# Kernel tuning notes

Measured on AMD Instinct MI355X. Metric: run time of the kernel, lower is better.

The kernel has to match this reference:

```python
import jax, jax.numpy as jnp
import numpy as np

SEQ, B, H = 2048, 2, 4096
N_HEADS = 32
N_KV = 2
HEAD_DIM = H // N_HEADS          # 128
ROT_DIM = HEAD_DIM // 2          # 64 (rope cache last-2 dim = 32 pairs)


def setup_inputs() -> dict:
    key = jax.random.key(0)
    ks = jax.random.split(key, 8)
    hidden_states = jax.random.normal(ks[0], (SEQ, B, H), dtype=jnp.float32)
    rotary_pos_emb = jax.random.normal(ks[1], (SEQ, 1, ROT_DIM // 2, 2), dtype=jnp.float32)
    s = 0.02
    Wq = jax.random.normal(ks[2], (H, H), dtype=jnp.float32) * s
    bq = jnp.zeros((H,), dtype=jnp.float32)
    Wk = jax.random.normal(ks[3], (H, N_KV * HEAD_DIM), dtype=jnp.float32) * s
    bk = jnp.zeros((N_KV * HEAD_DIM,), dtype=jnp.float32)
    Wv = jax.random.normal(ks[4], (H, N_KV * HEAD_DIM), dtype=jnp.float32) * s
    bv = jnp.zeros((N_KV * HEAD_DIM,), dtype=jnp.float32)
    Wo = jax.random.normal(ks[5], (H, H), dtype=jnp.float32) * s
    return {"hidden_states": hidden_states, "rotary_pos_emb": rotary_pos_emb,
            "Wq": Wq, "bq": bq, "Wk": Wk, "bk": bk, "Wv": Wv, "bv": bv, "Wo": Wo}


def _apply_rope(x, rope):
    # x: [sq, b, np, hn]; rope: [sq, 1, rot/2, 2]
    sq = x.shape[0]
    rot = rope.shape[-2] * 2
    x_rot, x_pass = x[..., :rot], x[..., rot:]
    xs = x_rot.reshape(x.shape[0], x.shape[1], x.shape[2], rot // 2, 2)
    rc = rope[:sq].reshape(sq, -1, 1, rot // 2, 2)  # [sq,1,1,rot/2,2]
    o0 = xs[..., 0] * rc[..., 0] - xs[..., 1] * rc[..., 1]
    o1 = xs[..., 1] * rc[..., 0] + xs[..., 0] * rc[..., 1]
    out = jnp.stack([o0, o1], axis=-1).reshape(x_rot.shape)
    return jnp.concatenate([out, x_pass], axis=-1)


def reference(hidden_states, rotary_pos_emb, Wq, bq, Wk, bk, Wv, bv, Wo):
    sq, b, h = hidden_states.shape
    group = N_HEADS // N_KV

    q = (hidden_states @ Wq + bq).reshape(sq, b, N_HEADS, HEAD_DIM)
    k = (hidden_states @ Wk + bk).reshape(sq, b, N_KV, HEAD_DIM)
    v = (hidden_states @ Wv + bv).reshape(sq, b, N_KV, HEAD_DIM)

    q = _apply_rope(q, rotary_pos_emb)
    k = _apply_rope(k, rotary_pos_emb)

    # GQA expand: head index = kv_head * group + g (matches expand+view in torch)
    k = jnp.repeat(k, group, axis=2)  # [sq, b, N_HEADS, hd]
    v = jnp.repeat(v, group, axis=2)

    scale = 1.0 / np.sqrt(HEAD_DIM)
    scores = jnp.einsum("sbhd,tbhd->bhst", q, k) * scale  # [b, nh, sq, sq]
    causal = jnp.tril(jnp.ones((sq, sq), dtype=bool))
    scores = jnp.where(causal, scores, jnp.finfo(scores.dtype).min)
    probs = jax.nn.softmax(scores, axis=-1)
    ctx = jnp.einsum("bhst,tbhd->sbhd", probs, v)  # [sq, b, nh, hd]
    ctx = ctx.reshape(sq, b, h)
    return ctx @ Wo
```

## Files before the change

### kernel.cpp

```cpp
#include <hip/hip_runtime.h>
#include <stdint.h>

#define SEQ   2048
#define BATCH 2
#define HD    4096
#define NH    32
#define NKV   2
#define HDIM  128
#define NT    (SEQ*BATCH)
#define KVC   (NKV*HDIM)

typedef short  bf16x8 __attribute__((ext_vector_type(8)));
typedef short  sh4    __attribute__((ext_vector_type(4)));
typedef float  f32x4  __attribute__((ext_vector_type(4)));

__device__ __forceinline__ float bf2f(unsigned short u){
  union { unsigned int i; float f; } v; v.i = ((unsigned int)u) << 16; return v.f;
}
__device__ __forceinline__ unsigned short f2bf(float f){
  union { float f; unsigned int i; } v; v.f = f;
  unsigned int r = v.i + 0x7FFFu + ((v.i >> 16) & 1u);
  return (unsigned short)(r >> 16);
}
__device__ __forceinline__ unsigned int cvtpk_bf16(float lo, float hi){
  unsigned int r;
  asm("v_cvt_pk_bf16_f32 %0, %1, %2" : "=v"(r) : "v"(lo), "v"(hi));
  return r;
}

__device__ __forceinline__ void gload_lds16(const void* g, void* lds){
  __builtin_amdgcn_global_load_lds(
      (const __attribute__((address_space(1))) unsigned int*)(size_t)g,
      (__attribute__((address_space(3))) unsigned int*)(unsigned int)(size_t)lds,
      16, 0, 0);
}

__device__ __forceinline__ void BARRIER(){
  __builtin_amdgcn_sched_barrier(0);
  asm volatile("" ::: "memory");
  __builtin_amdgcn_s_barrier();
  asm volatile("" ::: "memory");
  __builtin_amdgcn_sched_barrier(0);
}
#define VMCNT(N) do { asm volatile("s_waitcnt vmcnt(" #N ")" ::: "memory"); \
                      __builtin_amdgcn_sched_barrier(0); } while(0)

__global__ void k_cast(const float* __restrict__ in, unsigned short* __restrict__ out, int n4){
  int i = blockIdx.x * blockDim.x + threadIdx.x;
  if (i >= n4) return;
  float4 v = ((const float4*)in)[i];
  ushort4 o; o.x = f2bf(v.x); o.y = f2bf(v.y); o.z = f2bf(v.z); o.w = f2bf(v.w);
  ((ushort4*)out)[i] = o;
}

__global__ void k_transpose(const float* __restrict__ W, unsigned short* __restrict__ WT,
                            int K, int N){
  __shared__ float t[32][33];
  int n0 = blockIdx.x * 32, k0 = blockIdx.y * 32;
  int tx = threadIdx.x, ty = threadIdx.y;
  t[ty][tx] = W[(size_t)(k0 + ty) * N + n0 + tx];
  __syncthreads();
  WT[(size_t)(n0 + ty) * K + k0 + tx] = f2bf(t[tx][ty]);
}

template<bool OUTF32>
__global__ __launch_bounds__(256) void k_gemm(
    const unsigned short* __restrict__ A,
    const unsigned short* __restrict__ BT,
    const float* __restrict__ bias,
    const float* __restrict__ bias2, int bsplit,
    void* __restrict__ C, int M, int N, int K)
{
  __shared__ unsigned short As[128*32];
  __shared__ unsigned short Bs[128*32];
  const int tid  = threadIdx.x;
  const int lane = tid & 63;
  const int w    = tid >> 6;
  const int l4   = lane >> 4, l15 = lane & 15;
  const int wm   = (w >> 1) * 64, wn = (w & 1) * 64;
  const size_t bm = (size_t)blockIdx.y * 128, bn = (size_t)blockIdx.x * 128;

  f32x4 acc[4][4] = {};
  const int scol = (lane & 3) * 8;

  for (int k0 = 0; k0 < K; k0 += 32) {
    #pragma unroll
    for (int j = 0; j < 2; ++j) {
      const int r = w*32 + j*16 + (lane >> 2);
      gload_lds16(A  + (bm + r) * (size_t)K + k0 + scol, As + (size_t)(w*32 + j*16) * 32);
      gload_lds16(BT + (bn + r) * (size_t)K + k0 + scol, Bs + (size_t)(w*32 + j*16) * 32);
    }
    __syncthreads();
    bf16x8 af[4], bfr[4];
    #pragma unroll
    for (int m = 0; m < 4; ++m)
      af[m] = *(const bf16x8*)(As + (wm + m*16 + l15)*32 + l4*8);
    #pragma unroll
    for (int n = 0; n < 4; ++n)
      bfr[n] = *(const bf16x8*)(Bs + (wn + n*16 + l15)*32 + l4*8);
    #pragma unroll
    for (int m = 0; m < 4; ++m)
      #pragma unroll
      for (int n = 0; n < 4; ++n)
        acc[m][n] = __builtin_amdgcn_mfma_f32_16x16x32_bf16(af[m], bfr[n], acc[m][n], 0, 0, 0);
    __syncthreads();
  }

  #pragma unroll
  for (int n = 0; n < 4; ++n) {
    const size_t col = bn + wn + n*16 + l15;
    float badd = 0.0f;
    if (bias) badd = (bias2 && (int)col >= bsplit) ? bias2[col - bsplit] : bias[col];
    #pragma unroll
    for (int m = 0; m < 4; ++m) {
      const size_t row0 = bm + wm + m*16 + l4*4;
      #pragma unroll
      for (int r = 0; r < 4; ++r) {
        float v = acc[m][n][r] + badd;
        if (OUTF32) ((float*)C)[(row0 + r) * (size_t)N + col] = v;
        else ((unsigned short*)C)[(row0 + r) * (size_t)N + col] = f2bf(v);
      }
    }
  }
}

template<bool OUTF32>
__global__ __launch_bounds__(512, 2) void k_gemm256(
    const unsigned short* __restrict__ A,
    const unsigned short* __restrict__ BT,
    const float* __restrict__ bias,
    void* __restrict__ C, int M, int N, int K)
{
  __shared__ __attribute__((aligned(16))) unsigned short As[2][16384];
  __shared__ __attribute__((aligned(16))) unsigned short Bs[2][16384];
  const int tid  = threadIdx.x;
  const int lane = tid & 63;
  const int w    = tid >> 6;
  const int c    = lane & 15, g = lane >> 4;
  const int wm   = w >> 2, wn = w & 3;

  const int nwg = (int)(gridDim.x * gridDim.y);
  int bid = (int)(blockIdx.y * gridDim.x + blockIdx.x);
  if ((nwg & 7) == 0) bid = (bid & 7) * (nwg >> 3) + (bid >> 3);
  const int bx = bid % (int)gridDim.x, by = bid / (int)gridDim.x;
  const size_t bm = (size_t)by * 256, bn = (size_t)bx * 256;

  const char* Ab = (const char*)(A  + bm * (size_t)K);
  const char* Bb = (const char*)(BT + bn * (size_t)K);
  const size_t Kb2 = (size_t)K * 2;
  const int cswz = (c & 7) << 4;

  f32x4 acc[8][4] = {};
  bf16x8 af[4][2], bfr[4][2];

#define STAGE_A(bi, h, k0) do { \
    _Pragma("unroll") \
    for (int _j = 0; _j < 2; ++_j) { \
      const int _i = _j*512 + tid; \
      const int _row = (h)*128 + (_i >> 3); \
      const int _ch  = _i & 7; \
      gload_lds16(Ab + (size_t)_row * Kb2 + (size_t)(k0)*2 + ((_ch*16) ^ ((_row & 7) << 4)), \
                  (char*)As[bi] + (h)*16384 + _j*8192 + w*1024); \
    } } while(0)
#define STAGE_B(bi, h, k0) do { \
    _Pragma("unroll") \
    for (int _j = 0; _j < 2; ++_j) { \
      const int _i = _j*512 + tid; \
      const int _row = (h)*128 + (_i >> 3); \
      const int _ch  = _i & 7; \
      gload_lds16(Bb + (size_t)_row * Kb2 + (size_t)(k0)*2 + ((_ch*16) ^ ((_row & 7) << 4)), \
                  (char*)Bs[bi] + (h)*16384 + _j*8192 + w*1024); \
    } } while(0)
#define LDA(bi, mg) do { \
    _Pragma("unroll") \
    for (int _m = 0; _m < 4; ++_m) { \
      const char* _p = (const char*)As[bi] + (size_t)(((mg)*128 + _m*32 + wm*16 + c) * 128); \
      af[_m][0] = *(const bf16x8*)(_p + (( 0 + g*16) ^ cswz)); \
      af[_m][1] = *(const bf16x8*)(_p + ((64 + g*16) ^ cswz)); \
    } } while(0)
#define LDB(bi, ng) do { \
    _Pragma("unroll") \
    for (int _n = 0; _n < 2; ++_n) { \
      const char* _p = (const char*)Bs[bi] + (size_t)((((ng)*2+_n)*64 + wn*16 + c) * 128); \
      bfr[(ng)*2+_n][0] = *(const bf16x8*)(_p + (( 0 + g*16) ^ cswz)); \
      bfr[(ng)*2+_n][1] = *(const bf16x8*)(_p + ((64 + g*16) ^ cswz)); \
    } } while(0)
#define MFMA16(mg, ng) do { \
    __builtin_amdgcn_s_setprio(1); \
    _Pragma("unroll") \
    for (int _m = 0; _m < 4; ++_m) \
      _Pragma("unroll") \
      for (int _n = 0; _n < 2; ++_n) { \
        acc[(mg)*4+_m][(ng)*2+_n] = __builtin_amdgcn_mfma_f32_16x16x32_bf16( \
            af[_m][0], bfr[(ng)*2+_n][0], acc[(mg)*4+_m][(ng)*2+_n], 0, 0, 0); \
        acc[(mg)*4+_m][(ng)*2+_n] = __builtin_amdgcn_mfma_f32_16x16x32_bf16( \
            af[_m][1], bfr[(ng)*2+_n][1], acc[(mg)*4+_m][(ng)*2+_n], 0, 0, 0); \
      } \
    __builtin_amdgcn_s_setprio(0); \
  } while(0)

  STAGE_A(0, 0, 0);
  STAGE_B(0, 0, 0);
  STAGE_B(0, 1, 0);
  STAGE_A(0, 1, 0);
  STAGE_A(1, 0, 64);
  STAGE_B(1, 0, 64);
  VMCNT(8);
  BARRIER();

  const int niter = K >> 7;
  for (int it = 0; it < niter; ++it) {
    const int kb = it*128 + 64;
    int k2 = it*128 + 128; if (k2 >= K) k2 = 0;
    int k3 = it*128 + 192; if (k3 >= K) k3 = 0;
    LDA(0, 0); LDB(0, 0);
    STAGE_A(1, 1, kb);
    BARRIER();
    MFMA16(0, 0);
    VMCNT(6);
    BARRIER();
    LDB(0, 1);
    STAGE_B(1, 1, kb);
    BARRIER();
    MFMA16(0, 1);
    BARRIER();
    LDA(0, 1);
    STAGE_A(0, 0, k2);
    BARRIER();
    MFMA16(1, 0);
    BARRIER();
    STAGE_B(0, 0, k2);
    BARRIER();
    MFMA16(1, 1);
    VMCNT(8);
    BARRIER();
    LDA(1, 0); LDB(1, 0);
    STAGE_A(0, 1, k2);
    BARRIER();
    MFMA16(0, 0);
    VMCNT(6);
    BARRIER();
    LDB(1, 1);
    STAGE_B(0, 1, k2);
    BARRIER();
    MFMA16(0, 1);
    BARRIER();
    LDA(1, 1);
    STAGE_A(1, 0, k3);
    BARRIER();
    MFMA16(1, 0);
    BARRIER();
    STAGE_B(1, 0, k3);
    BARRIER();
    MFMA16(1, 1);
    VMCNT(8);
    BARRIER();
  }

  #pragma unroll
  for (int m = 0; m < 8; ++m) {
    const size_t row0 = bm + m*32 + wm*16 + g*4;
    #pragma unroll
    for (int n = 0; n < 4; ++n) {
      const size_t col = bn + n*64 + wn*16 + c;
      const float badd = bias ? bias[col] : 0.0f;
      #pragma unroll
      for (int r = 0; r < 4; ++r) {
        float v = acc[m][n][r] + badd;
        if (OUTF32) ((float*)C)[(row0 + r) * (size_t)N + col] = v;
        else ((unsigned short*)C)[(row0 + r) * (size_t)N + col] = f2bf(v);
      }
    }
  }
#undef STAGE_A
#undef STAGE_B
#undef LDA
#undef LDB
#undef MFMA16
}

__global__ void k_rope(const unsigned short* __restrict__ In, const float* __restrict__ rope,
                       unsigned short* __restrict__ Out, int ldin, int ncols, int nslab,
                       int psh, float sc)
{
  int idx = blockIdx.x * 256 + threadIdx.x;
  int npair = ncols >> 1;
  if (idx >= NT * npair) return;
  int t = idx >> psh, pr = idx & (npair - 1);
  int colp = pr * 2, h = colp >> 7, d = colp & 127;
  int s = t >> 1, b = t & 1;
  float x0 = bf2f(In[(size_t)t * ldin + colp]);
  float x1 = bf2f(In[(size_t)t * ldin + colp + 1]);
  float o0 = x0, o1 = x1;
  if (d < 64) {
    int i2 = d >> 1;
    float cr = rope[((size_t)s * 32 + i2) * 2 + 0];
    float ci = rope[((size_t)s * 32 + i2) * 2 + 1];
    o0 = x0 * cr - x1 * ci;
    o1 = x1 * cr + x0 * ci;
  }
  size_t dst = ((size_t)(b * nslab + h) * SEQ + s) * HDIM + d;
  Out[dst]     = f2bf(o0 * sc);
  Out[dst + 1] = f2bf(o1 * sc);
}

__global__ void k_vt(const unsigned short* __restrict__ In, int ld,
                     unsigned short* __restrict__ Out){
  int idx = blockIdx.x * 256 + threadIdx.x;
  if (idx >= NT * KVC) return;
  int t = idx >> 8, cp = idx & 255;
  int kv = cp >> 7, d = cp & 127;
  int s = t >> 1, b = t & 1;
  Out[((size_t)(b * NKV + kv) * HDIM + d) * SEQ + s] = In[(size_t)t * ld + cp];
}

__global__ __launch_bounds__(256) void k_attn(
    const unsigned short* __restrict__ Q,
    const unsigned short* __restrict__ Kk,
    const unsigned short* __restrict__ Vt,
    unsigned short* __restrict__ Ctx)
{
  const int tid  = threadIdx.x;
  const int lane = tid & 63;
  const int w    = tid >> 6;
  const int g = lane >> 4, c = lane & 15;
  const int bh = blockIdx.y;
  const int b = bh >> 5, h = bh & 31;
  const int qb  = (int)(gridDim.x - 1 - blockIdx.x);
  const int qw0 = qb * 64 + w * 16;

  const unsigned short* Qb = Q  + ((size_t)(b * NH  + h)        * SEQ + qw0) * HDIM;
  const char* Kb = (const char*)(Kk + ((size_t)(b * NKV + (h >> 4)) * SEQ) * HDIM);
  const char* Vb = (const char*)(Vt + ((size_t)(b * NKV + (h >> 4)) * HDIM) * SEQ);

  __shared__ unsigned short Ks[64*128];
  __shared__ unsigned short Vs[128*64];
  __shared__ unsigned short Pl[4][16 * 72];
  unsigned short* P = Pl[w];

  bf16x8 qf[4];
  #pragma unroll
  for (int kk = 0; kk < 4; ++kk)
    qf[kk] = *(const bf16x8*)(Qb + (size_t)c * HDIM + kk*32 + g*8);

  f32x4 of[8] = {};
  float mrun = -1e30f, lrun = 0.0f;
  const int qmax = qw0 + 15;
  const int tblk = qb * 64 + 64;

  const int kr = lane >> 4, kc = lane & 15;
  const int vr = lane >> 3, vc = lane & 7;
  const int swz = (c & 7) << 4;

  for (int t0 = 0; t0 < tblk; t0 += 64) {
    #pragma unroll
    for (int j = 0; j < 4; ++j) {
      const int r = w*16 + j*4 + kr;
      gload_lds16(Kb + (size_t)(t0 + r) * 256 + ((kc*16) ^ ((r & 7) << 4)),
                  (char*)Ks + (w*16 + j*4) * 256);
    }
    #pragma unroll
    for (int j = 0; j < 4; ++j) {
      const int d = w*32 + j*8 + vr;
      gload_lds16(Vb + (size_t)d * (SEQ*2) + (size_t)t0*2 + ((vc*16) ^ ((d & 7) << 4)),
                  (char*)Vs + (w*32 + j*8) * 128);
    }
    __syncthreads();

    f32x4 st[4];
    #pragma unroll
    for (int T = 0; T < 4; ++T) {
      if (t0 + T*16 <= qmax) {
        f32x4 s = {};
        #pragma unroll
        for (int kk = 0; kk < 4; ++kk) {
          bf16x8 kf = *(const bf16x8*)((const char*)Ks + (T*16 + c)*256 + ((kk*64 + g*16) ^ swz));
          s = __builtin_amdgcn_mfma_f32_16x16x32_bf16(kf, qf[kk], s, 0, 0, 0);
        }
        #pragma unroll
        for (int r = 0; r < 4; ++r) {
          const int t = t0 + T*16 + g*4 + r;
          if (t > qw0 + c) s[r] = -1e30f;
        }
        st[T] = s;
      } else {
        st[T] = (f32x4){-1e30f, -1e30f, -1e30f, -1e30f};
      }
    }
    float mloc = -1e30f;
    #pragma unroll
    for (int T = 0; T < 4; ++T)
      #pragma unroll
      for (int r = 0; r < 4; ++r)
        mloc = fmaxf(mloc, st[T][r]);
    mloc = fmaxf(mloc, __shfl_xor(mloc, 16));
    mloc = fmaxf(mloc, __shfl_xor(mloc, 32));
    if (!__all(mloc - mrun <= 8.0f)) {
      const float mn = fmaxf(mrun, mloc);
      const float al = exp2f(mrun - mn);
      mrun = mn;
      lrun *= al;
      float alr[4];
      #pragma unroll
      for (int r = 0; r < 4; ++r) alr[r] = __shfl(al, g*4 + r);
      #pragma unroll
      for (int d8 = 0; d8 < 8; ++d8)
        #pragma unroll
        for (int r = 0; r < 4; ++r)
          of[d8][r] *= alr[r];
    }
    float ps = 0.0f;
    #pragma unroll
    for (int T = 0; T < 4; ++T) {
      const float p0 = exp2f(st[T][0] - mrun);
      const float p1 = exp2f(st[T][1] - mrun);
      const float p2 = exp2f(st[T][2] - mrun);
      const float p3 = exp2f(st[T][3] - mrun);
      ps += (p0 + p1) + (p2 + p3);
      const unsigned int w0 = cvtpk_bf16(p0, p1);
      const unsigned int w1 = cvtpk_bf16(p2, p3);
      *(uint2*)(P + c*72 + T*16 + g*4) = make_uint2(w0, w1);
    }
    ps += __shfl_xor(ps, 16);
    ps += __shfl_xor(ps, 32);
    lrun += ps;

    asm volatile("s_waitcnt lgkmcnt(0)" ::: "memory");
    __builtin_amdgcn_sched_barrier(0);

    const bf16x8 pa0 = *(const bf16x8*)(P + c*72 + g*8);
    #pragma unroll
    for (int d8 = 0; d8 < 8; ++d8) {
      bf16x8 vf = *(const bf16x8*)((const char*)Vs + (d8*16 + c)*128 + ((g*16) ^ swz));
      of[d8] = __builtin_amdgcn_mfma_f32_16x16x32_bf16(pa0, vf, of[d8], 0, 0, 0);
    }
    if (t0 + 32 <= qmax) {
      const bf16x8 pa1 = *(const bf16x8*)(P + c*72 + 32 + g*8);
      #pragma unroll
      for (int d8 = 0; d8 < 8; ++d8) {
        bf16x8 vf = *(const bf16x8*)((const char*)Vs + (d8*16 + c)*128 + ((64 + g*16) ^ swz));
        of[d8] = __builtin_amdgcn_mfma_f32_16x16x32_bf16(pa1, vf, of[d8], 0, 0, 0);
      }
    }
    __syncthreads();
  }

  float lr[4];
  #pragma unroll
  for (int r = 0; r < 4; ++r) lr[r] = 1.0f / __shfl(lrun, g*4 + r);
  #pragma unroll
  for (int d8 = 0; d8 < 8; ++d8) {
    #pragma unroll
    for (int r = 0; r < 4; ++r) {
      const int s = qw0 + g*4 + r;
      const float v = of[d8][r] * lr[r];
      Ctx[((size_t)(s * BATCH + b)) * HD + (size_t)h * HDIM + d8*16 + c] = f2bf(v);
    }
  }
}

extern "C" void kernel_launch(void* const* d_in, const int* in_sizes, int n_in,
                              void* d_out, int out_size, void* d_ws, size_t ws_size,
                              hipStream_t stream)
{
  const float* hs   = (const float*)d_in[0];
  const float* rope = (const float*)d_in[1];
  const float* Wq   = (const float*)d_in[2];
  const float* bq   = (const float*)d_in[3];
  const float* Wk   = (const float*)d_in[4];
  const float* bk   = (const float*)d_in[5];
  const float* Wv   = (const float*)d_in[6];
  const float* bv   = (const float*)d_in[7];
  const float* Wo   = (const float*)d_in[8];

  char* ws = (char*)d_ws;
  const size_t MB = (size_t)1 << 20;
  unsigned short* Xbf  = (unsigned short*)(ws);
  unsigned short* Ctx  = Xbf;
  unsigned short* WqT  = (unsigned short*)(ws + 32*MB);
  unsigned short* Qa   = WqT;
  unsigned short* WkT  = (unsigned short*)(ws + 64*MB);
  unsigned short* WvT  = (unsigned short*)(ws + 66*MB);
  unsigned short* WoT  = (unsigned short*)(ws + 68*MB);
  unsigned short* Qtmp = (unsigned short*)(ws + 100*MB);
  unsigned short* KVt  = (unsigned short*)(ws + 132*MB);
  unsigned short* Ka   = (unsigned short*)(ws + 136*MB);
  unsigned short* VTa  = (unsigned short*)(ws + 138*MB);

  k_cast<<<(NT*HD/4 + 255)/256, 256, 0, stream>>>(hs, Xbf, NT*HD/4);

  dim3 tb(32, 32);
  k_transpose<<<dim3(HD/32,  HD/32), tb, 0, stream>>>(Wq, WqT, HD, HD);
  k_transpose<<<dim3(KVC/32, HD/32), tb, 0, stream>>>(Wk, WkT, HD, KVC);
  k_transpose<<<dim3(KVC/32, HD/32), tb, 0, stream>>>(Wv, WvT, HD, KVC);
  k_transpose<<<dim3(HD/32,  HD/32), tb, 0, stream>>>(Wo, WoT, HD, HD);

  k_gemm256<false><<<dim3(HD/256, NT/256), 512, 0, stream>>>(Xbf, WqT, bq, Qtmp, NT, HD, HD);
  k_gemm<false><<<dim3(512/128, NT/128), 256, 0, stream>>>(Xbf, WkT, bk, bv, 256,
                                                           KVt, NT, 512, HD);

  const float scq = 0.08838834764831845f * 1.4426950408889634f;
  k_rope<<<(NT*(HD/2)  + 255)/256, 256, 0, stream>>>(Qtmp, rope, Qa, HD, HD, NH, 11, scq);
  k_rope<<<(NT*(KVC/2) + 255)/256, 256, 0, stream>>>(KVt, rope, Ka, 512, KVC, NKV, 7, 1.0f);
  k_vt  <<<(NT*KVC     + 255)/256, 256, 0, stream>>>(KVt + 256, 512, VTa);

  k_attn<<<dim3(SEQ/64, NH*BATCH), 256, 0, stream>>>(Qa, Ka, VTa, Ctx);

  k_gemm256<true><<<dim3(HD/256, NT/256), 512, 0, stream>>>(Ctx, WoT, nullptr, d_out, NT, HD, HD);
}
```

Baseline: 665.5 us.

## Rewrite attention with 32x32 MFMA tiles and register-resident P via permlane swap

The attention kernel moves from 16x16x32 to 32x32x16 bf16 MFMA. Each wave now owns 32 query rows and each block 128, which halves the grid and doubles K/V reuse per tile load. The softmax probabilities are packed and rearranged in registers with v_permlane32_swap instead of a round trip through LDS, and the row max needs fewer shuffles. This removes the P shared buffer and its waitcnt, at the cost of more registers, fewer blocks for the causal workload to balance across, and a launch bound of 2 blocks per CU.

New measurement: 604.3 us. 9.2% less time.

```diff
diff --git a/kernel.cpp b/kernel.cpp
--- a/kernel.cpp
+++ b/kernel.cpp
@@ -13,6 +13,7 @@
 typedef short  bf16x8 __attribute__((ext_vector_type(8)));
 typedef short  sh4    __attribute__((ext_vector_type(4)));
 typedef float  f32x4  __attribute__((ext_vector_type(4)));
+typedef float  f32x16 __attribute__((ext_vector_type(16)));
 
 __device__ __forceinline__ float bf2f(unsigned short u){
   union { unsigned int i; float f; } v; v.i = ((unsigned int)u) << 16; return v.f;
@@ -26,6 +27,21 @@
   unsigned int r;
   asm("v_cvt_pk_bf16_f32 %0, %1, %2" : "=v"(r) : "v"(lo), "v"(hi));
   return r;
+}
+__device__ __forceinline__ void plane_swap(unsigned int &a, unsigned int &b){
+  asm("v_permlane32_swap_b32 %0, %1" : "+v"(a), "+v"(b));
+}
+__device__ __forceinline__ bf16x8 mk_pf(float a0f,float a1f,float a2f,float a3f,
+                                        float b0f,float b1f,float b2f,float b3f){
+  unsigned int a0 = cvtpk_bf16(a0f, a1f);
+  unsigned int a1 = cvtpk_bf16(a2f, a3f);
+  unsigned int b0 = cvtpk_bf16(b0f, b1f);
+  unsigned int b1 = cvtpk_bf16(b2f, b3f);
+  plane_swap(a0, b0);
+  plane_swap(a1, b1);
+  union { unsigned int u[4]; bf16x8 h; } u;
+  u.u[0] = a0; u.u[1] = a1; u.u[2] = b0; u.u[3] = b1;
+  return u.h;
 }
 
 __device__ __forceinline__ void gload_lds16(const void* g, void* lds){
@@ -314,7 +330,7 @@
   Out[((size_t)(b * NKV + kv) * HDIM + d) * SEQ + s] = In[(size_t)t * ld + cp];
 }
 
-__global__ __launch_bounds__(256) void k_attn(
+__global__ __launch_bounds__(256, 2) void k_attn(
     const unsigned short* __restrict__ Q,
     const unsigned short* __restrict__ Kk,
     const unsigned short* __restrict__ Vt,
@@ -323,11 +339,12 @@
   const int tid  = threadIdx.x;
   const int lane = tid & 63;
   const int w    = tid >> 6;
-  const int g = lane >> 4, c = lane & 15;
+  const int l31  = lane & 31;
+  const int hi   = lane >> 5;
   const int bh = blockIdx.y;
   const int b = bh >> 5, h = bh & 31;
   const int qb  = (int)(gridDim.x - 1 - blockIdx.x);
-  const int qw0 = qb * 64 + w * 16;
+  const int qw0 = qb * 128 + w * 32;
 
   const unsigned short* Qb = Q  + ((size_t)(b * NH  + h)        * SEQ + qw0) * HDIM;
   const char* Kb = (const char*)(Kk + ((size_t)(b * NKV + (h >> 4)) * SEQ) * HDIM);
@@ -335,22 +352,21 @@
 
   __shared__ unsigned short Ks[64*128];
   __shared__ unsigned short Vs[128*64];
-  __shared__ unsigned short Pl[4][16 * 72];
-  unsigned short* P = Pl[w];
-
-  bf16x8 qf[4];
+
+  bf16x8 qf[8];
   #pragma unroll
-  for (int kk = 0; kk < 4; ++kk)
-    qf[kk] = *(const bf16x8*)(Qb + (size_t)c * HDIM + kk*32 + g*8);
-
-  f32x4 of[8] = {};
+  for (int kk = 0; kk < 8; ++kk)
+    qf[kk] = *(const bf16x8*)(Qb + (size_t)l31 * HDIM + kk*16 + hi*8);
+
+  f32x16 of0 = {}, of1 = {}, of2 = {}, of3 = {};
   float mrun = -1e30f, lrun = 0.0f;
-  const int qmax = qw0 + 15;
-  const int tblk = qb * 64 + 64;
+  const int qmax = qw0 + 31;
+  const int qg   = qw0 + l31;
+  const int tblk = qb * 128 + 128;
 
   const int kr = lane >> 4, kc = lane & 15;
   const int vr = lane >> 3, vc = lane & 7;
-  const int swz = (c & 7) << 4;
+  const int rswz = (l31 & 7) << 4;
 
   for (int t0 = 0; t0 < tblk; t0 += 64) {
     #pragma unroll
@@ -367,96 +383,107 @@
     }
     __syncthreads();
 
-    f32x4 st[4];
-    #pragma unroll
-    for (int T = 0; T < 4; ++T) {
-      if (t0 + T*16 <= qmax) {
-        f32x4 s = {};
+    if (t0 <= qmax) {
+      f32x16 s0 = {};
+      #pragma unroll
+      for (int kk = 0; kk < 8; ++kk) {
+        bf16x8 kf = *(const bf16x8*)((const char*)Ks + l31*256 + ((kk*32 + hi*16) ^ rswz));
+        s0 = __builtin_amdgcn_mfma_f32_32x32x16_bf16(kf, qf[kk], s0, 0, 0, 0);
+      }
+      const int qh0 = qg - t0 - 4*hi;
+      if (t0 + 31 > qw0) {
         #pragma unroll
-        for (int kk = 0; kk < 4; ++kk) {
-          bf16x8 kf = *(const bf16x8*)((const char*)Ks + (T*16 + c)*256 + ((kk*64 + g*16) ^ swz));
-          s = __builtin_amdgcn_mfma_f32_16x16x32_bf16(kf, qf[kk], s, 0, 0, 0);
+        for (int r = 0; r < 16; ++r) {
+          const int tc = (r & 3) + 8*(r >> 2);
+          if (tc > qh0) s0[r] = -1e30f;
         }
+      }
+      const bool act1 = (t0 + 32 <= qmax);
+      f32x16 s1 = {};
+      if (act1) {
         #pragma unroll
-        for (int r = 0; r < 4; ++r) {
-          const int t = t0 + T*16 + g*4 + r;
-          if (t > qw0 + c) s[r] = -1e30f;
+        for (int kk = 0; kk < 8; ++kk) {
+          bf16x8 kf = *(const bf16x8*)((const char*)Ks + (32 + l31)*256 + ((kk*32 + hi*16) ^ rswz));
+          s1 = __builtin_amdgcn_mfma_f32_32x32x16_bf16(kf, qf[kk], s1, 0, 0, 0);
         }
-        st[T] = s;
-      } else {
-        st[T] = (f32x4){-1e30f, -1e30f, -1e30f, -1e30f};
-      }
-    }
-    float mloc = -1e30f;
-    #pragma unroll
-    for (int T = 0; T < 4; ++T)
+        if (t0 + 63 > qw0) {
+          const int qh1 = qh0 - 32;
+          #pragma unroll
+          for (int r = 0; r < 16; ++r) {
+            const int tc = (r & 3) + 8*(r >> 2);
+            if (tc > qh1) s1[r] = -1e30f;
+          }
+        }
+      }
+      float mloc = s0[0];
       #pragma unroll
-      for (int r = 0; r < 4; ++r)
-        mloc = fmaxf(mloc, st[T][r]);
-    mloc = fmaxf(mloc, __shfl_xor(mloc, 16));
-    mloc = fmaxf(mloc, __shfl_xor(mloc, 32));
-    if (!__all(mloc - mrun <= 8.0f)) {
-      const float mn = fmaxf(mrun, mloc);
-      const float al = exp2f(mrun - mn);
-      mrun = mn;
-      lrun *= al;
-      float alr[4];
+      for (int r = 1; r < 16; ++r) mloc = fmaxf(mloc, s0[r]);
+      if (act1) {
+        #pragma unroll
+        for (int r = 0; r < 16; ++r) mloc = fmaxf(mloc, s1[r]);
+      }
+      mloc = fmaxf(mloc, __shfl_xor(mloc, 32));
+      if (!__all(mloc - mrun <= 8.0f)) {
+        const float mn = fmaxf(mrun, mloc);
+        const float al = exp2f(mrun - mn);
+        mrun = mn;
+        lrun *= al;
+        of0 *= al; of1 *= al; of2 *= al; of3 *= al;
+      }
+      float ps = 0.0f;
+      float p0[16];
       #pragma unroll
-      for (int r = 0; r < 4; ++r) alr[r] = __shfl(al, g*4 + r);
-      #pragma unroll
-      for (int d8 = 0; d8 < 8; ++d8)
+      for (int r = 0; r < 16; ++r) { p0[r] = exp2f(s0[r] - mrun); ps += p0[r]; }
+      const bf16x8 pf0 = mk_pf(p0[0],p0[1],p0[2],p0[3],   p0[4],p0[5],p0[6],p0[7]);
+      const bf16x8 pf1 = mk_pf(p0[8],p0[9],p0[10],p0[11], p0[12],p0[13],p0[14],p0[15]);
+      bf16x8 pf2, pf3;
+      if (act1) {
+        float p1[16];
         #pragma unroll
-        for (int r = 0; r < 4; ++r)
-          of[d8][r] *= alr[r];
-    }
-    float ps = 0.0f;
-    #pragma unroll
-    for (int T = 0; T < 4; ++T) {
-      const float p0 = exp2f(st[T][0] - mrun);
-      const float p1 = exp2f(st[T][1] - mrun);
-      const float p2 = exp2f(st[T][2] - mrun);
-      const float p3 = exp2f(st[T][3] - mrun);
-      ps += (p0 + p1) + (p2 + p3);
-      const unsigned int w0 = cvtpk_bf16(p0, p1);
-      const unsigned int w1 = cvtpk_bf16(p2, p3);
-      *(uint2*)(P + c*72 + T*16 + g*4) = make_uint2(w0, w1);
-    }
-    ps += __shfl_xor(ps, 16);
-    ps += __shfl_xor(ps, 32);
-    lrun += ps;
-
-    asm volatile("s_waitcnt lgkmcnt(0)" ::: "memory");
-    __builtin_amdgcn_sched_barrier(0);
-
-    const bf16x8 pa0 = *(const bf16x8*)(P + c*72 + g*8);
-    #pragma unroll
-    for (int d8 = 0; d8 < 8; ++d8) {
-      bf16x8 vf = *(const bf16x8*)((const char*)Vs + (d8*16 + c)*128 + ((g*16) ^ swz));
-      of[d8] = __builtin_amdgcn_mfma_f32_16x16x32_bf16(pa0, vf, of[d8], 0, 0, 0);
-    }
-    if (t0 + 32 <= qmax) {
-      const bf16x8 pa1 = *(const bf16x8*)(P + c*72 + 32 + g*8);
-      #pragma unroll
-      for (int d8 = 0; d8 < 8; ++d8) {
-        bf16x8 vf = *(const bf16x8*)((const char*)Vs + (d8*16 + c)*128 + ((64 + g*16) ^ swz));
-        of[d8] = __builtin_amdgcn_mfma_f32_16x16x32_bf16(pa1, vf, of[d8], 0, 0, 0);
-      }
+        for (int r = 0; r < 16; ++r) { p1[r] = exp2f(s1[r] - mrun); ps += p1[r]; }
+        pf2 = mk_pf(p1[0],p1[1],p1[2],p1[3],   p1[4],p1[5],p1[6],p1[7]);
+        pf3 = mk_pf(p1[8],p1[9],p1[10],p1[11], p1[12],p1[13],p1[14],p1[15]);
+      }
+      ps += __shfl_xor(ps, 32);
+      lrun += ps;
+
+#define PVDT(ofv, dt) do { \
+        const char* _vrow = (const char*)Vs + (size_t)(((dt)*32 + l31) * 128); \
+        bf16x8 _v0 = *(const bf16x8*)(_vrow + (( 0 + hi*16) ^ rswz)); \
+        bf16x8 _v1 = *(const bf16x8*)(_vrow + ((32 + hi*16) ^ rswz)); \
+        ofv = __builtin_amdgcn_mfma_f32_32x32x16_bf16(_v0, pf0, ofv, 0, 0, 0); \
+        ofv = __builtin_amdgcn_mfma_f32_32x32x16_bf16(_v1, pf1, ofv, 0, 0, 0); \
+        if (act1) { \
+          bf16x8 _v2 = *(const bf16x8*)(_vrow + ((64 + hi*16) ^ rswz)); \
+          bf16x8 _v3 = *(const bf16x8*)(_vrow + ((96 + hi*16) ^ rswz)); \
+          ofv = __builtin_amdgcn_mfma_f32_32x32x16_bf16(_v2, pf2, ofv, 0, 0, 0); \
+          ofv = __builtin_amdgcn_mfma_f32_32x32x16_bf16(_v3, pf3, ofv, 0, 0, 0); \
+        } } while(0)
+      PVDT(of0, 0);
+      PVDT(of1, 1);
+      PVDT(of2, 2);
+      PVDT(of3, 3);
+#undef PVDT
     }
     __syncthreads();
   }
 
-  float lr[4];
-  #pragma unroll
-  for (int r = 0; r < 4; ++r) lr[r] = 1.0f / __shfl(lrun, g*4 + r);
-  #pragma unroll
-  for (int d8 = 0; d8 < 8; ++d8) {
-    #pragma unroll
-    for (int r = 0; r < 4; ++r) {
-      const int s = qw0 + g*4 + r;
-      const float v = of[d8][r] * lr[r];
-      Ctx[((size_t)(s * BATCH + b)) * HD + (size_t)h * HDIM + d8*16 + c] = f2bf(v);
-    }
-  }
+  const float inv = 1.0f / lrun;
+  unsigned short* Crow = Ctx + ((size_t)(qg * BATCH + b)) * HD + (size_t)h * HDIM;
+#define EPI(ofv, dt) do { \
+    _Pragma("unroll") \
+    for (int _q = 0; _q < 4; ++_q) { \
+      const int _col = (dt)*32 + 8*_q + 4*hi; \
+      const unsigned int _w0 = cvtpk_bf16(ofv[4*_q+0]*inv, ofv[4*_q+1]*inv); \
+      const unsigned int _w1 = cvtpk_bf16(ofv[4*_q+2]*inv, ofv[4*_q+3]*inv); \
+      *(unsigned int*)(Crow + _col)     = _w0; \
+      *(unsigned int*)(Crow + _col + 2) = _w1; \
+    } } while(0)
+  EPI(of0, 0);
+  EPI(of1, 1);
+  EPI(of2, 2);
+  EPI(of3, 3);
+#undef EPI
 }
 
 extern "C" void kernel_launch(void* const* d_in, const int* in_sizes, int n_in,
@@ -504,7 +531,7 @@
   k_rope<<<(NT*(KVC/2) + 255)/256, 256, 0, stream>>>(KVt, rope, Ka, 512, KVC, NKV, 7, 1.0f);
   k_vt  <<<(NT*KVC     + 255)/256, 256, 0, stream>>>(KVt + 256, 512, VTa);
 
-  k_attn<<<dim3(SEQ/64, NH*BATCH), 256, 0, stream>>>(Qa, Ka, VTa, Ctx);
+  k_attn<<<dim3(SEQ/128, NH*BATCH), 256, 0, stream>>>(Qa, Ka, VTa, Ctx);
 
   k_gemm256<true><<<dim3(HD/256, NT/256), 512, 0, stream>>>(Ctx, WoT, nullptr, d_out, NT, HD, HD);
 }
```
